# Kernel optimization log

Measured on AMD Instinct MI355X. Metric: run time of the kernel, lower is better.

The kernel has to match this reference:

```python
import jax, jax.numpy as jnp
import numpy as np

# ---- constants hardcoded in the original source ----
N_RBF = 50            # number of RBF policy centers
n = 4                 # cartpole state dim [x, xdot, theta, thetadot]
H = 60                # rollout horizon (hardcoded inside get_future_reward)
DT = 0.05             # dt_outer
KAPPA = 1.0           # UT spread parameter
JITTER = 1e-6
PROC_NOISE = 1e-2     # per-step process noise variance
# dynamics_params = [polemass_length, gravity, length, masspole, total_mass]
PML, G, LEN, MP, MT = 0.05, 9.8, 0.5, 0.1, 1.1

_diag_idx = np.arange(n)
_lr, _lc = np.tril_indices(n, -1)


def _build_L(sp):
    # sp: (N_RBF, n + n(n-1)/2) -> lower-triangular Cholesky factors (N_RBF, n, n)
    L = jnp.zeros((N_RBF, n, n), sp.dtype)
    L = L.at[:, _diag_idx, _diag_idx].set(sp[:, :n])
    L = L.at[:, _lr, _lc].set(sp[:, n:])
    return L


def _policy(params, x):
    # RBF policy: u = sum_i w_i * exp(-(x-mu_i)^T L_i L_i^T (x-mu_i)), clipped to force limits
    w = params[:N_RBF]
    mu = params[N_RBF:N_RBF + n * N_RBF].reshape(n, N_RBF)
    L = _build_L(params[N_RBF + n * N_RBF:].reshape(N_RBF, n + (n * n - n) // 2))
    d = x[:, None] - mu                          # (n, N)
    Ld = jnp.einsum('Nkj,kN->Nj', L, d)          # L_i^T d_i  -> (N, n)
    phi = jnp.exp(-jnp.sum(Ld * Ld, axis=1))     # (N,)
    return jnp.clip(jnp.dot(w, phi), -10.0, 10.0)


def _dyn(x, u):
    # gym cartpole continuous dynamics; x: (4, P) columns of sigma points
    pos, vel, th, thd = x
    s, c = jnp.sin(th), jnp.cos(th)
    temp = (u + PML * thd ** 2 * s) / MT
    thacc = (G * s - c * temp) / (LEN * (4.0 / 3.0 - MP * c * c / MT))
    xacc = temp - PML * thacc * c / MT
    return jnp.stack([vel, xacc, thd, thacc])


def _ut_weights(dtype):
    w0 = KAPPA / (n + KAPPA)
    wi = 1.0 / (2.0 * (n + KAPPA))
    return jnp.concatenate([jnp.array([w0], dtype), jnp.full((2 * n,), wi, dtype)])


def _gen_sigma(mu, cov):
    # standard unscented-transform sigma points from (mu, cov)
    S = jnp.linalg.cholesky(cov + JITTER * jnp.eye(n, dtype=mu.dtype))
    root = jnp.sqrt(n + KAPPA) * S               # (n, n)
    pts = jnp.concatenate([mu[:, None], mu[:, None] + root, mu[:, None] - root], axis=1)  # (n, 2n+1)
    return pts, _ut_weights(mu.dtype)


def _reward(states, weights):
    # quadratic cost UT-mean evaluator
    pos, vel, th, thd = states
    cost = pos ** 2 + vel ** 2 + 10.0 * th ** 2 + thd ** 2
    return -jnp.dot(weights, cost)


def _rollout(params, x0):
    states, weights = _gen_sigma(x0, jnp.zeros((n, n), x0.dtype))  # initialize sigma points at x0

    def body(carry, _):
        states, weights = carry                       # (4, 9), (9,)
        mean = states @ weights                        # UT mean
        u = _policy(params, mean)
        # sigma_point_expand: propagate each point, expand with process-noise UT points
        next_means = states + DT * _dyn(states, u)     # (4, 9)
        cov = PROC_NOISE * DT * jnp.eye(n, dtype=x0.dtype)
        S = jnp.linalg.cholesky(cov + JITTER * jnp.eye(n, dtype=x0.dtype))
        root = jnp.sqrt(n + KAPPA) * S
        offsets = jnp.concatenate([jnp.zeros((n, 1), x0.dtype), root, -root], axis=1)  # (4, 9)
        exp_states = (next_means[:, :, None] + offsets[:, None, :]).reshape(n, -1)      # (4, 81)
        ut_w = _ut_weights(x0.dtype)
        exp_weights = (weights[:, None] * ut_w[None, :]).reshape(-1)                    # (81,)
        # sigma_point_compress: moment-match and regenerate 2n+1 points
        m = exp_states @ exp_weights
        d = exp_states - m[:, None]
        covc = (d * exp_weights) @ d.T
        states, weights = _gen_sigma(m, covc)
        return (states, weights), _reward(states, weights)

    _, rewards = jax.lax.scan(body, (states, weights), None, length=H)
    return jnp.sum(rewards)


def setup_inputs() -> dict:
    key = jax.random.key(0)
    num_params = N_RBF + n * N_RBF + N_RBF * (n + (n * n - n) // 2)  # 750
    param = jax.random.normal(key, (num_params,), jnp.float32) * 0.1
    return {"param": param}


def reference(param):
    x0 = jnp.array([0.0, 0.0, 0.1, 0.0], param.dtype)
    return _rollout(param, x0)
```

## Files before the change

kernel.cpp:

```cpp
#include <hip/hip_runtime.h>
#include <math.h>


template <int CTRL>
__device__ __forceinline__ float dpp_add_f(float v) {
    int s = __builtin_amdgcn_update_dpp(0, __float_as_int(v), CTRL, 0xF, 0xF, true);
    return v + __int_as_float(s);
}
__device__ __forceinline__ float row_sum_f(float v) {
    v = dpp_add_f<0xB1>(v);
    v = dpp_add_f<0x4E>(v);
    v = dpp_add_f<0x124>(v);
    v = dpp_add_f<0x128>(v);
    return v;
}
__device__ __forceinline__ float rl(float v, int lane) {
    return __int_as_float(__builtin_amdgcn_readlane(__float_as_int(v), lane));
}
__device__ __forceinline__ float wave_sum_f(float v) {
    v = row_sum_f(v);
    v = dpp_add_f<0x142>(v);
    v = dpp_add_f<0x143>(v);
    return rl(v, 63);
}

__global__ __launch_bounds__(64) void horizon_kernel(const float* __restrict__ p,
                                                     float* __restrict__ out) {
    const int l   = threadIdx.x;
    const int l15 = l & 15;
    const bool r1 = (l >> 4) & 1, r2 = (l >> 4) & 2;

    const float SQL2E  = 1.2011224087864498f;
    const float INV_MT = 0.9090909090909091f;
    const float KCS    = -0.045454545454545456f;
    const double INV2PI_D = 0.15915494309189535;
    const float  INV2PI_F = 0.15915494309189535f;
    const float DIAG5  = 0.00251f;

    float w = 0.0f, mu0 = 0.0f, mu1 = 0.0f, mu2 = 0.0f, mu3 = 0.0f;
    float s0=0,s1=0,s2=0,s3=0,s4=0,s5=0,s6=0,s7=0,s8=0,s9=0;
    if (l < 50) {
        w   = p[l];
        mu0 = p[ 50 + l]; mu1 = p[100 + l]; mu2 = p[150 + l]; mu3 = p[200 + l];
        const float* q = p + 250 + 10 * l;
        s0 = q[0]*SQL2E; s1 = q[1]*SQL2E; s2 = q[2]*SQL2E; s3 = q[3]*SQL2E;
        s4 = q[4]*SQL2E; s5 = q[5]*SQL2E; s6 = q[6]*SQL2E; s7 = q[7]*SQL2E;
        s8 = q[8]*SQL2E; s9 = q[9]*SQL2E;
    }

    const float wlf  = (l15 == 0) ? 0.2f : ((l15 < 9) ? 0.1f : 0.0f);
    const float fw5  = 5.0f * wlf;
    const float osgn = (l15 >= 1 && l15 <= 4) ? 1.0f
                     : ((l15 >= 5 && l15 <= 8) ? -1.0f : 0.0f);
    const int   ocol = ((l15 >= 5 ? l15 - 5 : l15 - 1) & 3);

    float mmf0 = 0.0f, mmf1 = 0.0f, mmf2 = 0.1f, mmf3 = 0.0f;
    float d0 = -mu0, d1 = -mu1, d2 = 0.1f - mu2, d3 = -mu3;
    double rev = 0.1 * INV2PI_D;
    float frmf = (float)rev;
    const float CI = 2.2360679774997896e-3f;
    float c00=CI, c10=0.f, c20=0.f, c30=0.f;
    float c11=CI, c21=0.f, c31=0.f;
    float c22=CI, c32=0.f;
    float c33=CI;
    float acc = 0.0f;

    #pragma unroll 2
    for (int t = 0; t < 60; ++t) {
        float oo0 = osgn * ((ocol == 0) ? c00 : 0.0f);
        float oo1 = osgn * ((ocol == 0) ? c10 : ((ocol == 1) ? c11 : 0.0f));
        float oo2 = osgn * ((ocol == 0) ? c20 : ((ocol == 1) ? c21 :
                            ((ocol == 2) ? c22 : 0.0f)));
        float oo3 = osgn * ((ocol == 0) ? c30 : ((ocol == 1) ? c31 :
                            ((ocol == 2) ? c32 : c33)));

        float x1 = mmf1 + oo1;
        float x3 = mmf3 + oo3;

        float rv = __builtin_amdgcn_fractf(fmaf(oo2, INV2PI_F, frmf));
        float sn = __builtin_amdgcn_sinf(rv);
        float cs = __builtin_amdgcn_cosf(rv);
        float a   = (0.045454545454545456f * (x3 * x3)) * sn;
        float den = fmaf(cs * cs, KCS, 0.6666666666666666f);
        float rden = __builtin_amdgcn_rcpf(den);
        float g0 = fmaf(9.8f, sn, -(cs * a)) * rden;
        float g1 = (-INV_MT) * (cs * rden);
        float kcs = KCS * cs;
        float h0 = fmaf(kcs, g0, a);
        float h1 = fmaf(kcs, g1, INV_MT);
        float al1 = fmaf(0.05f, h0, oo1), be1 = 0.05f * h1;
        float al3 = fmaf(0.05f, g0, oo3), be3 = 0.05f * g1;
        float dl0 = fmaf(0.05f, x1, oo0);
        float dl2 = fmaf(0.05f, x3, oo2);

        float selA = r1 ? (r2 ? al3 : al1) : (r2 ? dl2 : dl0);
        float PA = row_sum_f(wlf * selA);
        float A0 = rl(PA, 0), A1 = rl(PA, 16), A2 = rl(PA, 32), A3 = rl(PA, 48);
        float selB = r1 ? (r2 ? be3 : be1) : 0.0f;
        float PB = row_sum_f(wlf * selB);
        float B1 = rl(PB, 16), B3 = rl(PB, 48);

        float v0 = dl0 - A0, v2 = dl2 - A2;
        float va1 = al1 - A1, vb1 = be1 - B1;
        float va3 = al3 - A3, vb3 = be3 - B3;
        float sa = r1 ? v2 : v0;
        sa = r2 ? (r1 ? 0.0f : v2) : sa;
        float sb = r2 ? v2 : v0;
        float P1 = row_sum_f((fw5 * sa) * sb);
        float A00 = rl(P1, 0) + DIAG5, A20 = rl(P1, 16), A22 = rl(P1, 32) + DIAG5;
        float i0 = __builtin_amdgcn_rsqf(A00);
        float nc00 = A00 * i0;
        float nc20 = A20 * i0;
        float b22p = fmaf(-nc20, nc20, A22);

        float nmm0 = mmf0 + A0, nmm2 = mmf2 + A2;
        double revn = fma((double)A2, INV2PI_D, rev);
        rev = revn - floor(revn);
        float nfrm = (float)rev;

        float t0p = fmaf(s0, d0, s5 * d2);
        float t1p = s6 * d2;
        float t2p = s2 * d2;
        float t0v = fmaf(s4, d1, fmaf(s7, d3, t0p));
        float t1v = fmaf(s1, d1, fmaf(s8, d3, t1p));
        float t2v = fmaf(s9, d3, t2p);
        float t3v = s3 * d3;
        float qn = fmaf(t0v, t0v, fmaf(t1v, t1v, fmaf(t2v, t2v, t3v * t3v)));
        float val = wave_sum_f(w * __builtin_amdgcn_exp2f(-qn));
        float u = fminf(10.0f, fmaxf(-10.0f, val));

        float rd1 = fmaf(B1, u, A1);
        float rd3 = fmaf(B3, u, A3);
        d0 += A0; d2 += A2; d1 += rd1; d3 += rd3;
        float nmm1 = mmf1 + rd1, nmm3 = mmf3 + rd3;

        float v1 = fmaf(vb1, u, va1);
        float v3 = fmaf(vb3, u, va3);
        float lo2 = r2 ? v2 : v0, hi2 = r2 ? v3 : v1;
        float P2 = row_sum_f((fw5 * v1) * (r1 ? hi2 : lo2));
        float s3a = r1 ? v2 : v0;
        s3a = r2 ? (r1 ? 0.0f : v3) : s3a;
        float P3 = row_sum_f((fw5 * v3) * s3a);
        float A10 = rl(P2, 0), A11 = rl(P2, 16) + DIAG5;
        float A21 = rl(P2, 32), A31 = rl(P2, 48);
        float A30 = rl(P3, 0), A32 = rl(P3, 16), A33 = rl(P3, 32) + DIAG5;

        float rwm = fmaf(nmm0, nmm0, fmaf(nmm1, nmm1,
                    fmaf(10.0f * nmm2, nmm2, nmm3 * nmm3)));
        float rwa = A00 + A11 + 10.0f * A22 + A33;
        acc -= fmaf(0.2f, rwa, rwm);

        float nc10 = A10 * i0;
        float nc30 = A30 * i0;
        float b11 = fmaf(-nc10, nc10, A11);
        float i1 = __builtin_amdgcn_rsqf(b11);
        float nc11 = b11 * i1;
        float nc21 = fmaf(-nc20, nc10, A21) * i1;
        float nc31 = fmaf(-nc30, nc10, A31) * i1;
        float b22 = fmaf(-nc21, nc21, b22p);
        float i2 = __builtin_amdgcn_rsqf(b22);
        float nc22 = b22 * i2;
        float nc32 = fmaf(-nc31, nc21, fmaf(-nc30, nc20, A32)) * i2;
        float b33 = fmaf(-nc32, nc32, fmaf(-nc31, nc31, fmaf(-nc30, nc30, A33)));
        float nc33 = b33 * __builtin_amdgcn_rsqf(b33);

        c00 = nc00; c10 = nc10; c20 = nc20; c30 = nc30;
        c11 = nc11; c21 = nc21; c31 = nc31;
        c22 = nc22; c32 = nc32; c33 = nc33;
        mmf0 = nmm0; mmf1 = nmm1; mmf2 = nmm2; mmf3 = nmm3;
        frmf = nfrm;
    }

    if (l == 0) out[0] = acc;
}

extern "C" void kernel_launch(void* const* d_in, const int* in_sizes, int n_in,
                              void* d_out, int out_size, void* d_ws, size_t ws_size,
                              hipStream_t stream) {
    (void)in_sizes; (void)n_in; (void)out_size; (void)d_ws; (void)ws_size;
    const float* p = (const float*)d_in[0];
    float* out = (float*)d_out;
    hipLaunchKernelGGL(horizon_kernel, dim3(1), dim3(64), 0, stream, p, out);
}
```

Baseline: 74.39 us.

## Restructure moment matching into u-independent second moments computed off critical path

The UT propagation is reorganized to use 8-lane groups. Deviations are taken relative to the centre sigma point, which is now computed separately per lane, and all second moments of the affine-in-u quantities are accumulated before the policy output u is known. Mean and covariance are then assembled as polynomials in u, which removes the reductions that used to wait on u. This trades more ALU work, an extra centre dynamics evaluation and more readlanes for a shorter dependency chain per step. Numerics change slightly because the moments are centred on the centre point rather than the mean.

```diff
diff --git a/kernel.cpp b/kernel.cpp
--- a/kernel.cpp
+++ b/kernel.cpp
@@ -14,6 +14,12 @@
     v = dpp_add_f<0x128>(v);
     return v;
 }
+__device__ __forceinline__ float row_sum8_f(float v) {
+    v = dpp_add_f<0xB1>(v);
+    v = dpp_add_f<0x4E>(v);
+    v = dpp_add_f<0x141>(v);
+    return v;
+}
 __device__ __forceinline__ float rl(float v, int lane) {
     return __int_as_float(__builtin_amdgcn_readlane(__float_as_int(v), lane));
 }
@@ -26,9 +32,9 @@
 
 __global__ __launch_bounds__(64) void horizon_kernel(const float* __restrict__ p,
                                                      float* __restrict__ out) {
-    const int l   = threadIdx.x;
-    const int l15 = l & 15;
-    const bool r1 = (l >> 4) & 1, r2 = (l >> 4) & 2;
+    const int l = threadIdx.x;
+    const int k = l & 7;
+    const int r = l >> 3;
 
     const float SQL2E  = 1.2011224087864498f;
     const float INV_MT = 0.9090909090909091f;
@@ -48,11 +54,18 @@
         s8 = q[8]*SQL2E; s9 = q[9]*SQL2E;
     }
 
-    const float wlf  = (l15 == 0) ? 0.2f : ((l15 < 9) ? 0.1f : 0.0f);
-    const float fw5  = 5.0f * wlf;
-    const float osgn = (l15 >= 1 && l15 <= 4) ? 1.0f
-                     : ((l15 >= 5 && l15 <= 8) ? -1.0f : 0.0f);
-    const int   ocol = ((l15 >= 5 ? l15 - 5 : l15 - 1) & 3);
+    const float osgn = (k < 4) ? 1.0f : -1.0f;
+    const int   ocol = k & 3;
+
+    const bool rb0  = (r & 1) != 0;
+    const bool rb1v = (r & 2) != 0;
+    const bool rb2v = (r & 4) != 0;
+    const bool hi67 = (r >= 6);
+    const bool lt5  = (r < 5);
+    const bool r7q  = (r == 7);
+    const bool r0q  = (r == 0);
+    const bool r2q  = (r == 2);
+    const bool rle2 = (r <= 2);
 
     float mmf0 = 0.0f, mmf1 = 0.0f, mmf2 = 0.1f, mmf3 = 0.0f;
     float d0 = -mu0, d1 = -mu1, d2 = 0.1f - mu2, d3 = -mu3;
@@ -67,6 +80,23 @@
 
     #pragma unroll 2
     for (int t = 0; t < 60; ++t) {
+        float snc = __builtin_amdgcn_sinf(frmf);
+        float csc = __builtin_amdgcn_cosf(frmf);
+        float a_c  = (0.045454545454545456f * (mmf3 * mmf3)) * snc;
+        float denc = fmaf(csc * csc, KCS, 0.6666666666666666f);
+        float rdc  = __builtin_amdgcn_rcpf(denc);
+        float g0c = fmaf(9.8f, snc, -(csc * a_c)) * rdc;
+        float g1c = (-INV_MT) * (csc * rdc);
+        float kcsc = KCS * csc;
+        float h0c = fmaf(kcsc, g0c, a_c);
+        float h1c = fmaf(kcsc, g1c, INV_MT);
+        float fac = 0.05f * mmf1;
+        float fbc = 0.05f * h0c;
+        float fcc = 0.05f * h1c;
+        float fdc = 0.05f * mmf3;
+        float fec = 0.05f * g0c;
+        float ffc = 0.05f * g1c;
+
         float oo0 = osgn * ((ocol == 0) ? c00 : 0.0f);
         float oo1 = osgn * ((ocol == 0) ? c10 : ((ocol == 1) ? c11 : 0.0f));
         float oo2 = osgn * ((ocol == 0) ? c20 : ((ocol == 1) ? c21 :
@@ -76,7 +106,6 @@
 
         float x1 = mmf1 + oo1;
         float x3 = mmf3 + oo3;
-
         float rv = __builtin_amdgcn_fractf(fmaf(oo2, INV2PI_F, frmf));
         float sn = __builtin_amdgcn_sinf(rv);
         float cs = __builtin_amdgcn_cosf(rv);
@@ -88,35 +117,12 @@
         float kcs = KCS * cs;
         float h0 = fmaf(kcs, g0, a);
         float h1 = fmaf(kcs, g1, INV_MT);
-        float al1 = fmaf(0.05f, h0, oo1), be1 = 0.05f * h1;
-        float al3 = fmaf(0.05f, g0, oo3), be3 = 0.05f * g1;
-        float dl0 = fmaf(0.05f, x1, oo0);
-        float dl2 = fmaf(0.05f, x3, oo2);
-
-        float selA = r1 ? (r2 ? al3 : al1) : (r2 ? dl2 : dl0);
-        float PA = row_sum_f(wlf * selA);
-        float A0 = rl(PA, 0), A1 = rl(PA, 16), A2 = rl(PA, 32), A3 = rl(PA, 48);
-        float selB = r1 ? (r2 ? be3 : be1) : 0.0f;
-        float PB = row_sum_f(wlf * selB);
-        float B1 = rl(PB, 16), B3 = rl(PB, 48);
-
-        float v0 = dl0 - A0, v2 = dl2 - A2;
-        float va1 = al1 - A1, vb1 = be1 - B1;
-        float va3 = al3 - A3, vb3 = be3 - B3;
-        float sa = r1 ? v2 : v0;
-        sa = r2 ? (r1 ? 0.0f : v2) : sa;
-        float sb = r2 ? v2 : v0;
-        float P1 = row_sum_f((fw5 * sa) * sb);
-        float A00 = rl(P1, 0) + DIAG5, A20 = rl(P1, 16), A22 = rl(P1, 32) + DIAG5;
-        float i0 = __builtin_amdgcn_rsqf(A00);
-        float nc00 = A00 * i0;
-        float nc20 = A20 * i0;
-        float b22p = fmaf(-nc20, nc20, A22);
-
-        float nmm0 = mmf0 + A0, nmm2 = mmf2 + A2;
-        double revn = fma((double)A2, INV2PI_D, rev);
-        rev = revn - floor(revn);
-        float nfrm = (float)rev;
+        float fa = fmaf(0.05f, x1, oo0);
+        float fb = fmaf(0.05f, h0, oo1);
+        float fc_ = 0.05f * h1;
+        float fd = fmaf(0.05f, x3, oo2);
+        float fe = fmaf(0.05f, g0, oo3);
+        float ff_ = 0.05f * g1;
 
         float t0p = fmaf(s0, d0, s5 * d2);
         float t1p = s6 * d2;
@@ -129,39 +135,124 @@
         float val = wave_sum_f(w * __builtin_amdgcn_exp2f(-qn));
         float u = fminf(10.0f, fmaxf(-10.0f, val));
 
+        float da = fa - fac, db = fb - fbc, dc_ = fc_ - fcc;
+        float dd = fd - fdc, de = fe - fec, df_ = ff_ - ffc;
+        float ha = 0.5f * da, hb = 0.5f * db, hc = 0.5f * dc_;
+        float hd = 0.5f * dd, he = 0.5f * de, hf = 0.5f * df_;
+
+        float c1a = rb0 ? hb : ha;
+        float c1b = rb0 ? hd : hc;
+        float c1c = rb0 ? hf : he;
+        float c1m0 = rb1v ? c1b : c1a;
+        float c1m1 = rb1v ? c1a : c1c;
+        float xs1 = rb2v ? c1m1 : c1m0;
+        float ys1 = hi67 ? 1.0f : da;
+        float sr1 = row_sum8_f(xs1 * ys1);
+
+        float c2a = rb0 ? hc : hb;
+        float c2b = rb0 ? he : hd;
+        float c2c = rb0 ? hc : hf;
+        float c2m0 = rb1v ? c2b : c2a;
+        float c2m1 = rb1v ? c2b : c2c;
+        float xs2 = rb2v ? c2m1 : c2m0;
+        float ys2 = lt5 ? db : 1.0f;
+        float sr2 = row_sum8_f(xs2 * ys2);
+
+        float c3a = rb0 ? hd : hc;
+        float c3b = rb0 ? hf : he;
+        float c3c = rb0 ? he : hd;
+        float c3m0 = rb1v ? c3b : c3a;
+        float c3m1 = rb1v ? hf  : c3c;
+        float xs3 = rb2v ? c3m1 : c3m0;
+        float ys3 = rb2v ? (r7q ? 1.0f : dd) : dc_;
+        float sr3 = row_sum8_f(xs3 * ys3);
+
+        float xs4 = r2q ? hf : he;
+        float ys4 = r0q ? de : (rle2 ? df_ : 0.0f);
+        float sr4 = row_sum8_f(xs4 * ys4);
+
+        float SAA = rl(sr1,  0), SAB = rl(sr1,  8), SAC = rl(sr1, 16);
+        float SAD = rl(sr1, 24), SAE = rl(sr1, 32), SAF = rl(sr1, 40);
+        float SmA = rl(sr1, 48), SmB = rl(sr1, 56);
+        float SBB = rl(sr2,  0), SBC = rl(sr2,  8), SBD = rl(sr2, 16);
+        float SBE = rl(sr2, 24), SBF = rl(sr2, 32);
+        float SmC = rl(sr2, 40), SmD = rl(sr2, 48), SmE = rl(sr2, 56);
+        float SCC = rl(sr3,  0), SCD = rl(sr3,  8), SCE = rl(sr3, 16);
+        float SCF = rl(sr3, 24), SDD = rl(sr3, 32), SDE = rl(sr3, 40);
+        float SDF = rl(sr3, 48), SmF = rl(sr3, 56);
+        float SEE = rl(sr4,  0), SEF = rl(sr4,  8), SFF = rl(sr4, 16);
+
+        float muA = 0.2f * SmA, muB = 0.2f * SmB, muC = 0.2f * SmC;
+        float muD = 0.2f * SmD, muE = 0.2f * SmE, muF = 0.2f * SmF;
+        float A0 = fac + muA;
+        float A1 = fbc + muB;
+        float B1 = fcc + muC;
+        float A2 = fdc + muD;
+        float A3 = fec + muE;
+        float B3 = ffc + muF;
+
+        float CAA = fmaf(-SmA, muA, SAA);
+        float CAB = fmaf(-SmA, muB, SAB);
+        float CAC = fmaf(-SmA, muC, SAC);
+        float CAD = fmaf(-SmA, muD, SAD);
+        float CAE = fmaf(-SmA, muE, SAE);
+        float CAF = fmaf(-SmA, muF, SAF);
+        float CBB = fmaf(-SmB, muB, SBB);
+        float CBC = fmaf(-SmB, muC, SBC);
+        float CBD = fmaf(-SmB, muD, SBD);
+        float CBE = fmaf(-SmB, muE, SBE);
+        float CBF = fmaf(-SmB, muF, SBF);
+        float CCC = fmaf(-SmC, muC, SCC);
+        float CCD = fmaf(-SmC, muD, SCD);
+        float CCE = fmaf(-SmC, muE, SCE);
+        float CCF = fmaf(-SmC, muF, SCF);
+        float CDD = fmaf(-SmD, muD, SDD);
+        float CDE = fmaf(-SmD, muE, SDE);
+        float CDF = fmaf(-SmD, muF, SDF);
+        float CEE = fmaf(-SmE, muE, SEE);
+        float CEF = fmaf(-SmE, muF, SEF);
+        float CFF = fmaf(-SmF, muF, SFF);
+
+        float E00 = CAA + DIAG5;
+        float E10 = fmaf(CAC, u, CAB);
+        float E11 = fmaf(fmaf(CCC, u, CBC + CBC), u, CBB) + DIAG5;
+        float E20 = CAD;
+        float E21 = fmaf(CCD, u, CBD);
+        float E22 = CDD + DIAG5;
+        float E30 = fmaf(CAF, u, CAE);
+        float E31 = fmaf(fmaf(CCF, u, CBF + CCE), u, CBE);
+        float E32 = fmaf(CDF, u, CDE);
+        float E33 = fmaf(fmaf(CFF, u, CEF + CEF), u, CEE) + DIAG5;
+
         float rd1 = fmaf(B1, u, A1);
         float rd3 = fmaf(B3, u, A3);
         d0 += A0; d2 += A2; d1 += rd1; d3 += rd3;
-        float nmm1 = mmf1 + rd1, nmm3 = mmf3 + rd3;
-
-        float v1 = fmaf(vb1, u, va1);
-        float v3 = fmaf(vb3, u, va3);
-        float lo2 = r2 ? v2 : v0, hi2 = r2 ? v3 : v1;
-        float P2 = row_sum_f((fw5 * v1) * (r1 ? hi2 : lo2));
-        float s3a = r1 ? v2 : v0;
-        s3a = r2 ? (r1 ? 0.0f : v3) : s3a;
-        float P3 = row_sum_f((fw5 * v3) * s3a);
-        float A10 = rl(P2, 0), A11 = rl(P2, 16) + DIAG5;
-        float A21 = rl(P2, 32), A31 = rl(P2, 48);
-        float A30 = rl(P3, 0), A32 = rl(P3, 16), A33 = rl(P3, 32) + DIAG5;
+        float nmm0 = mmf0 + A0, nmm1 = mmf1 + rd1;
+        float nmm2 = mmf2 + A2, nmm3 = mmf3 + rd3;
+        double revn = fma((double)A2, INV2PI_D, rev);
+        rev = revn - floor(revn);
+        float nfrm = (float)rev;
 
         float rwm = fmaf(nmm0, nmm0, fmaf(nmm1, nmm1,
                     fmaf(10.0f * nmm2, nmm2, nmm3 * nmm3)));
-        float rwa = A00 + A11 + 10.0f * A22 + A33;
+        float rwa = E00 + E11 + 10.0f * E22 + E33;
         acc -= fmaf(0.2f, rwa, rwm);
 
-        float nc10 = A10 * i0;
-        float nc30 = A30 * i0;
-        float b11 = fmaf(-nc10, nc10, A11);
+        float i0 = __builtin_amdgcn_rsqf(E00);
+        float nc00 = E00 * i0;
+        float nc10 = E10 * i0;
+        float nc20 = E20 * i0;
+        float nc30 = E30 * i0;
+        float b11 = fmaf(-nc10, nc10, E11);
         float i1 = __builtin_amdgcn_rsqf(b11);
         float nc11 = b11 * i1;
-        float nc21 = fmaf(-nc20, nc10, A21) * i1;
-        float nc31 = fmaf(-nc30, nc10, A31) * i1;
-        float b22 = fmaf(-nc21, nc21, b22p);
+        float nc21 = fmaf(-nc20, nc10, E21) * i1;
+        float nc31 = fmaf(-nc30, nc10, E31) * i1;
+        float b22 = fmaf(-nc21, nc21, fmaf(-nc20, nc20, E22));
         float i2 = __builtin_amdgcn_rsqf(b22);
         float nc22 = b22 * i2;
-        float nc32 = fmaf(-nc31, nc21, fmaf(-nc30, nc20, A32)) * i2;
-        float b33 = fmaf(-nc32, nc32, fmaf(-nc31, nc31, fmaf(-nc30, nc30, A33)));
+        float nc32 = fmaf(-nc31, nc21, fmaf(-nc30, nc20, E32)) * i2;
+        float b33 = fmaf(-nc32, nc32, fmaf(-nc31, nc31, fmaf(-nc30, nc30, E33)));
         float nc33 = b33 * __builtin_amdgcn_rsqf(b33);
 
         c00 = nc00; c10 = nc10; c20 = nc20; c30 = nc30;
```

Result: slower. 83.01 us (+11.6%).

## Simplify UT moment math analytically and restructure RBF distance with packed FMAs

Applied to the files above, without the earlier changes.

Linear components of the propagated mean (position and angle increments) are now computed in closed form from the previous mean, not via a lane reduction. The PA/PB reductions are merged into one row sum, and the first covariance block uses a shorter 8-lane reduction. Sigma lanes are reordered so the centre point sits at lane 8. The RBF quadratic form is rewritten as precomputed offsets plus packed v2f FMAs on the mean, replacing the tracked d vectors. The aim is a shorter serial dependency chain per horizon step, at the cost of changed floating-point rounding order.

```diff
diff --git a/kernel.cpp b/kernel.cpp
--- a/kernel.cpp
+++ b/kernel.cpp
@@ -1,6 +1,8 @@
 #include <hip/hip_runtime.h>
 #include <math.h>
 
+
+typedef float v2f __attribute__((ext_vector_type(2)));
 
 template <int CTRL>
 __device__ __forceinline__ float dpp_add_f(float v) {
@@ -14,6 +16,12 @@
     v = dpp_add_f<0x128>(v);
     return v;
 }
+__device__ __forceinline__ float row_sum8_f(float v) {
+    v = dpp_add_f<0xB1>(v);
+    v = dpp_add_f<0x4E>(v);
+    v = dpp_add_f<0x141>(v);
+    return v;
+}
 __device__ __forceinline__ float rl(float v, int lane) {
     return __int_as_float(__builtin_amdgcn_readlane(__float_as_int(v), lane));
 }
@@ -29,6 +37,7 @@
     const int l   = threadIdx.x;
     const int l15 = l & 15;
     const bool r1 = (l >> 4) & 1, r2 = (l >> 4) & 2;
+    const bool rbOr = r1 || r2;
 
     const float SQL2E  = 1.2011224087864498f;
     const float INV_MT = 0.9090909090909091f;
@@ -48,14 +57,25 @@
         s8 = q[8]*SQL2E; s9 = q[9]*SQL2E;
     }
 
-    const float wlf  = (l15 == 0) ? 0.2f : ((l15 < 9) ? 0.1f : 0.0f);
+    const float C0 = s0*mu0 + s4*mu1 + s5*mu2 + s7*mu3;
+    const float C1 = s1*mu1 + s6*mu2 + s8*mu3;
+    const float C2 = s2*mu2 + s9*mu3;
+    const float C3 = s3*mu3;
+    const v2f kA0 = {s0, 0.0f};
+    const v2f kA1 = {s4, s1};
+    const v2f kA2 = {s5, s6};
+    const v2f kA3 = {s7, s8};
+    const v2f kB2 = {s2, 0.0f};
+    const v2f kB3 = {s9, s3};
+    const v2f cA  = {-C0, -C1};
+    const v2f cB  = {-C2, -C3};
+
+    const float wlf  = (l15 < 8) ? 0.1f : ((l15 == 8) ? 0.2f : 0.0f);
     const float fw5  = 5.0f * wlf;
-    const float osgn = (l15 >= 1 && l15 <= 4) ? 1.0f
-                     : ((l15 >= 5 && l15 <= 8) ? -1.0f : 0.0f);
-    const int   ocol = ((l15 >= 5 ? l15 - 5 : l15 - 1) & 3);
+    const float osgn = (l15 < 4) ? 1.0f : ((l15 < 8) ? -1.0f : 0.0f);
+    const int   ocol = l15 & 3;
 
     float mmf0 = 0.0f, mmf1 = 0.0f, mmf2 = 0.1f, mmf3 = 0.0f;
-    float d0 = -mu0, d1 = -mu1, d2 = 0.1f - mu2, d3 = -mu3;
     double rev = 0.1 * INV2PI_D;
     float frmf = (float)rev;
     const float CI = 2.2360679774997896e-3f;
@@ -74,7 +94,6 @@
         float oo3 = osgn * ((ocol == 0) ? c30 : ((ocol == 1) ? c31 :
                             ((ocol == 2) ? c32 : c33)));
 
-        float x1 = mmf1 + oo1;
         float x3 = mmf3 + oo3;
 
         float rv = __builtin_amdgcn_fractf(fmaf(oo2, INV2PI_F, frmf));
@@ -90,57 +109,61 @@
         float h1 = fmaf(kcs, g1, INV_MT);
         float al1 = fmaf(0.05f, h0, oo1), be1 = 0.05f * h1;
         float al3 = fmaf(0.05f, g0, oo3), be3 = 0.05f * g1;
-        float dl0 = fmaf(0.05f, x1, oo0);
-        float dl2 = fmaf(0.05f, x3, oo2);
-
-        float selA = r1 ? (r2 ? al3 : al1) : (r2 ? dl2 : dl0);
+
+        float v0 = fmaf(0.05f, oo1, oo0);
+        float v2 = fmaf(0.05f, oo3, oo2);
+        float A2 = 0.05f * mmf3;
+
+        float selA = r2 ? (r1 ? be3 : be1) : (r1 ? al3 : al1);
         float PA = row_sum_f(wlf * selA);
-        float A0 = rl(PA, 0), A1 = rl(PA, 16), A2 = rl(PA, 32), A3 = rl(PA, 48);
-        float selB = r1 ? (r2 ? be3 : be1) : 0.0f;
-        float PB = row_sum_f(wlf * selB);
-        float B1 = rl(PB, 16), B3 = rl(PB, 48);
-
-        float v0 = dl0 - A0, v2 = dl2 - A2;
-        float va1 = al1 - A1, vb1 = be1 - B1;
-        float va3 = al3 - A3, vb3 = be3 - B3;
-        float sa = r1 ? v2 : v0;
-        sa = r2 ? (r1 ? 0.0f : v2) : sa;
-        float sb = r2 ? v2 : v0;
-        float P1 = row_sum_f((fw5 * sa) * sb);
-        float A00 = rl(P1, 0) + DIAG5, A20 = rl(P1, 16), A22 = rl(P1, 32) + DIAG5;
+        float q0 = fw5 * v0, q2 = fw5 * v2;
+        float xb = r2 ? q2 : q0;
+        float yb = rbOr ? v2 : v0;
+        float PB = row_sum8_f(xb * yb);
+
+        float A1 = rl(PA, 0), A3 = rl(PA, 16), B1 = rl(PA, 32), B3 = rl(PA, 48);
+        float A00 = rl(PB, 0) + DIAG5, A20 = rl(PB, 16), A22 = rl(PB, 32) + DIAG5;
+
         float i0 = __builtin_amdgcn_rsqf(A00);
         float nc00 = A00 * i0;
         float nc20 = A20 * i0;
         float b22p = fmaf(-nc20, nc20, A22);
 
-        float nmm0 = mmf0 + A0, nmm2 = mmf2 + A2;
+        float va1 = al1 - A1, vb1 = be1 - B1;
+        float va3 = al3 - A3, vb3 = be3 - B3;
+
+        float nmm0 = fmaf(0.05f, mmf1, mmf0), nmm2 = fmaf(0.05f, mmf3, mmf2);
         double revn = fma((double)A2, INV2PI_D, rev);
         rev = revn - floor(revn);
         float nfrm = (float)rev;
 
-        float t0p = fmaf(s0, d0, s5 * d2);
-        float t1p = s6 * d2;
-        float t2p = s2 * d2;
-        float t0v = fmaf(s4, d1, fmaf(s7, d3, t0p));
-        float t1v = fmaf(s1, d1, fmaf(s8, d3, t1p));
-        float t2v = fmaf(s9, d3, t2p);
-        float t3v = s3 * d3;
-        float qn = fmaf(t0v, t0v, fmaf(t1v, t1v, fmaf(t2v, t2v, t3v * t3v)));
+        v2f mS;
+        mS = (v2f){mmf3, mmf3};
+        v2f pt  = __builtin_elementwise_fma(kA3, mS, cA);
+        v2f pt2 = __builtin_elementwise_fma(kB3, mS, cB);
+        mS = (v2f){mmf2, mmf2};
+        pt  = __builtin_elementwise_fma(kA2, mS, pt);
+        pt2 = __builtin_elementwise_fma(kB2, mS, pt2);
+        mS = (v2f){mmf1, mmf1};
+        pt  = __builtin_elementwise_fma(kA1, mS, pt);
+        mS = (v2f){mmf0, mmf0};
+        pt  = __builtin_elementwise_fma(kA0, mS, pt);
+        v2f pq = pt * pt;
+        pq = __builtin_elementwise_fma(pt2, pt2, pq);
+        float qn = pq.x + pq.y;
         float val = wave_sum_f(w * __builtin_amdgcn_exp2f(-qn));
-        float u = fminf(10.0f, fmaxf(-10.0f, val));
+        float u = __builtin_amdgcn_fmed3f(val, -10.0f, 10.0f);
 
         float rd1 = fmaf(B1, u, A1);
         float rd3 = fmaf(B3, u, A3);
-        d0 += A0; d2 += A2; d1 += rd1; d3 += rd3;
         float nmm1 = mmf1 + rd1, nmm3 = mmf3 + rd3;
 
         float v1 = fmaf(vb1, u, va1);
         float v3 = fmaf(vb3, u, va3);
         float lo2 = r2 ? v2 : v0, hi2 = r2 ? v3 : v1;
         float P2 = row_sum_f((fw5 * v1) * (r1 ? hi2 : lo2));
-        float s3a = r1 ? v2 : v0;
-        s3a = r2 ? (r1 ? 0.0f : v3) : s3a;
-        float P3 = row_sum_f((fw5 * v3) * s3a);
+        float yw = r2 ? v3 : (r1 ? v2 : v0);
+        float P3 = row_sum_f((fw5 * v3) * yw);
         float A10 = rl(P2, 0), A11 = rl(P2, 16) + DIAG5;
         float A21 = rl(P2, 32), A31 = rl(P2, 48);
         float A30 = rl(P3, 0), A32 = rl(P3, 16), A33 = rl(P3, 32) + DIAG5;
```

Measured after the change: 70.94 us. -4.6%, faster.
